# Kernel optimization log

Hardware: AMD Instinct MI355X
Metric: run time of the kernel (lower is better)

## Reference

```python
import jax, jax.numpy as jnp
import numpy as np

DIN = 128
HID = 128
B, N = 32, 2048
NEG = 9000000000000000.0


def setup_inputs() -> dict:
    key = jax.random.key(0)
    ks = jax.random.split(key, 8)
    x = jax.random.normal(ks[0], (B, N, DIN), dtype=jnp.float32)
    mask = jax.random.randint(ks[1], (B, N, N), 0, 2).astype(jnp.float32)
    s = 1.0 / np.sqrt(DIN)
    Wv = jax.random.uniform(ks[2], (DIN, HID), minval=-s, maxval=s, dtype=jnp.float32)
    bv = jax.random.uniform(ks[3], (HID,), minval=-s, maxval=s, dtype=jnp.float32)
    Wk = jax.random.uniform(ks[4], (DIN, HID), minval=-s, maxval=s, dtype=jnp.float32)
    bk = jax.random.uniform(ks[5], (HID,), minval=-s, maxval=s, dtype=jnp.float32)
    Wq = jax.random.uniform(ks[6], (DIN, HID), minval=-s, maxval=s, dtype=jnp.float32)
    bq = jax.random.uniform(ks[7], (HID,), minval=-s, maxval=s, dtype=jnp.float32)
    return {"x": x, "mask": mask, "Wv": Wv, "bv": bv, "Wk": Wk, "bk": bk, "Wq": Wq, "bq": bq}


def reference(x, mask, Wv, bv, Wk, bk, Wq, bq):
    v = jnp.tanh(x @ Wv + bv)            # [B, N, H]
    q = jnp.tanh(x @ Wq + bq)            # [B, N, H]
    k = jnp.tanh(x @ Wk + bk)            # [B, N, H]
    scores = jnp.einsum('bih,bjh->bij', q, k)  # [B, N, N]
    scores = scores * mask - NEG * (1.0 - mask)
    att = jax.nn.softmax(scores, axis=-1)
    out = jnp.einsum('bij,bjh->bih', att, v)   # [B, N, H]
    return out
```

## Files before the change

### kernel.cpp

```cpp
#include <hip/hip_runtime.h>

#define DIN 128
#define HID 128
#define BB  32
#define NN  2048
#define LOG2E 1.44269504088896340736f

typedef float  f32x4   __attribute__((ext_vector_type(4)));
typedef __bf16 bf16x4v __attribute__((ext_vector_type(4)));
typedef __bf16 bf16x8  __attribute__((ext_vector_type(8)));

__device__ __forceinline__ float tanh_fast(float x) {
  float e = __expf(2.0f * x);
  return 1.0f - 2.0f / (e + 1.0f);
}

__global__ __launch_bounds__(256) void wt_kernel(
    const float* __restrict__ Wq, const float* __restrict__ Wk,
    const float* __restrict__ Wv, __bf16* __restrict__ wt) {
  const float* W = (blockIdx.x == 0) ? Wq : (blockIdx.x == 1) ? Wk : Wv;
  __bf16* dst = wt + blockIdx.x * (DIN * HID);
  int t = threadIdx.x;
#pragma unroll
  for (int c = 0; c < 16; ++c) {
    int o = c * 1024 + t * 4;
    int d = o >> 7, h = o & 127;
    f32x4 v = *(const f32x4*)(W + d * HID + h);
    dst[(h + 0) * DIN + d] = (__bf16)v.x;
    dst[(h + 1) * DIN + d] = (__bf16)v.y;
    dst[(h + 2) * DIN + d] = (__bf16)v.z;
    dst[(h + 3) * DIN + d] = (__bf16)v.w;
  }
}

__global__ __launch_bounds__(256) void proj_kernel(
    const float* __restrict__ x, const __bf16* __restrict__ wt,
    const float* __restrict__ bq, const float* __restrict__ bk,
    const float* __restrict__ bv, __bf16* __restrict__ qbf,
    __bf16* __restrict__ kbf, __bf16* __restrict__ vtbf) {
  int tid = threadIdx.x;
  int lane = tid & 63, w = tid >> 6;
  int l15 = lane & 15, quad = lane >> 4;
  long i0 = (long)blockIdx.x * 64;

  bf16x8 bx[4][4];
#pragma unroll
  for (int nt = 0; nt < 4; ++nt) {
    const float* xp = x + (i0 + nt * 16 + l15) * DIN;
#pragma unroll
    for (int ks = 0; ks < 4; ++ks) {
      int d0 = ks * 32 + quad * 8;
      f32x4 a = *(const f32x4*)(xp + d0);
      f32x4 b = *(const f32x4*)(xp + d0 + 4);
      bf16x8 f;
      f[0] = (__bf16)a.x; f[1] = (__bf16)a.y; f[2] = (__bf16)a.z; f[3] = (__bf16)a.w;
      f[4] = (__bf16)b.x; f[5] = (__bf16)b.y; f[6] = (__bf16)b.z; f[7] = (__bf16)b.w;
      bx[nt][ks] = f;
    }
  }

#pragma unroll
  for (int p = 0; p < 2; ++p) {
    const __bf16* wtp = wt + p * DIN * HID;
    const float* bias = (p == 0) ? bq : bk;
    __bf16* outp = (p == 0) ? qbf : kbf;
#pragma unroll
    for (int nt = 0; nt < 8; ++nt) {
      int h0 = nt * 16 + l15;
      f32x4 acc = {0.f, 0.f, 0.f, 0.f};
#pragma unroll
      for (int ks = 0; ks < 4; ++ks) {
        bf16x8 wf = *(const bf16x8*)(wtp + (long)h0 * DIN + ks * 32 + quad * 8);
        acc = __builtin_amdgcn_mfma_f32_16x16x32_bf16(bx[w][ks], wf, acc, 0, 0, 0);
      }
      float bcol = bias[h0];
      long rowb = i0 + w * 16 + quad * 4;
#pragma unroll
      for (int r = 0; r < 4; ++r) {
        float val = tanh_fast(acc[r] + bcol);
        if (p == 0) val *= LOG2E;
        outp[(rowb + r) * HID + h0] = (__bf16)val;
      }
    }
  }

  {
    const __bf16* wtp = wt + 2 * DIN * HID;
    long bb = i0 >> 11;
    int nloc = (int)(i0 & 2047);
    long vbase = bb * (long)HID * NN;
#pragma unroll
    for (int s = 0; s < 2; ++s) {
      int hb = w * 32 + s * 16;
      bf16x8 af[4];
#pragma unroll
      for (int ks = 0; ks < 4; ++ks)
        af[ks] = *(const bf16x8*)(wtp + (long)(hb + l15) * DIN + ks * 32 + quad * 8);
      float bvr[4];
#pragma unroll
      for (int r = 0; r < 4; ++r) bvr[r] = bv[hb + quad * 4 + r];
#pragma unroll
      for (int nt = 0; nt < 4; ++nt) {
        f32x4 acc = {0.f, 0.f, 0.f, 0.f};
#pragma unroll
        for (int ks = 0; ks < 4; ++ks)
          acc = __builtin_amdgcn_mfma_f32_16x16x32_bf16(af[ks], bx[nt][ks], acc, 0, 0, 0);
        int hrow = hb + quad * 4;
        int ncol = nloc + nt * 16 + l15;
#pragma unroll
        for (int r = 0; r < 4; ++r) {
          float val = tanh_fast(acc[r] + bvr[r]);
          vtbf[vbase + (long)(hrow + r) * NN + ncol] = (__bf16)val;
        }
      }
    }
  }
}

#define KSTR 136
#define VSTR 72
#define PSTR 72

__global__ __launch_bounds__(512, 4) void attn_kernel(
    const __bf16* __restrict__ qbf, const __bf16* __restrict__ kbf,
    const __bf16* __restrict__ vtbf, const float* __restrict__ mask,
    float* __restrict__ out) {
  __shared__ __bf16 Ks[64 * KSTR];
  __shared__ __bf16 Vts[128 * VSTR];
  __shared__ __bf16 Pl[8 * 16 * PSTR];

  const int tid = threadIdx.x;
  const int lane = tid & 63, w = tid >> 6;
  const int l15 = lane & 15, quad = lane >> 4;
  const int bid = blockIdx.x;
  const int vb = (bid >> 3) | ((bid & 7) << 6);
  const int b = vb >> 4;
  const int i0 = (vb & 15) * 128;
  const long kvbase = (long)b * NN * HID;

  bf16x8 qf[4];
  {
    const __bf16* qp = qbf + kvbase + (long)(i0 + w * 16 + l15) * HID + quad * 8;
#pragma unroll
    for (int ks = 0; ks < 4; ++ks) qf[ks] = *(const bf16x8*)(qp + ks * 32);
  }

  const int krow = tid >> 4, kcol = (tid & 15) * 8;
  const int vrow = tid >> 3, vcol = (tid & 7) * 8;
  const __bf16* kg = kbf + kvbase + (long)krow * HID + kcol;
  const __bf16* vg = vtbf + (long)b * HID * NN + (long)vrow * NN + vcol;
  __bf16* ksd0 = Ks + krow * KSTR + kcol;
  __bf16* ksd1 = Ks + (krow + 32) * KSTR + kcol;
  __bf16* vsd0 = Vts + vrow * VSTR + vcol;
  __bf16* vsd1 = Vts + (vrow + 64) * VSTR + vcol;
  const float* mp = mask + ((long)b * NN + (i0 + w * 16 + l15)) * NN + quad * 4;
  __bf16* Pw = Pl + w * 16 * PSTR;

  f32x4 O[8];
#pragma unroll
  for (int i = 0; i < 8; ++i) O[i] = (f32x4){0.f, 0.f, 0.f, 0.f};
  float mrow = -1e30f, lrow = 0.0f;

  bf16x8 kr0 = *(const bf16x8*)(kg);
  bf16x8 kr1 = *(const bf16x8*)(kg + 32 * HID);
  bf16x8 vr0 = *(const bf16x8*)(vg);
  bf16x8 vr1 = *(const bf16x8*)(vg + (long)64 * NN);
  f32x4 mr[4];
#pragma unroll
  for (int t = 0; t < 4; ++t) mr[t] = *(const f32x4*)(mp + t * 16);
  *(bf16x8*)ksd0 = kr0; *(bf16x8*)ksd1 = kr1;
  *(bf16x8*)vsd0 = vr0; *(bf16x8*)vsd1 = vr1;
  unsigned mbits;
  {
    float mb = 0.f;
#pragma unroll
    for (int t = 0; t < 4; ++t)
#pragma unroll
      for (int r = 0; r < 4; ++r)
        mb = fmaf(mr[t][r], (float)(1u << (t * 4 + r)), mb);
    mbits = (unsigned)mb;
  }
  __syncthreads();

  for (int jt = 0; jt < 32; ++jt) {
    const int jn = (jt < 31) ? jt + 1 : 31;
    {
      const __bf16* kgn = kg + (long)jn * 64 * HID;
      kr0 = *(const bf16x8*)(kgn);
      kr1 = *(const bf16x8*)(kgn + 32 * HID);
      const __bf16* vgn = vg + jn * 64;
      vr0 = *(const bf16x8*)(vgn);
      vr1 = *(const bf16x8*)(vgn + (long)64 * NN);
#pragma unroll
      for (int t = 0; t < 4; ++t) mr[t] = *(const f32x4*)(mp + jn * 64 + t * 16);
    }

    f32x4 pt[4];
#pragma unroll
    for (int t = 0; t < 4; ++t) {
      f32x4 acc = {0.f, 0.f, 0.f, 0.f};
      const __bf16* kp = Ks + (t * 16 + l15) * KSTR + quad * 8;
#pragma unroll
      for (int ks = 0; ks < 4; ++ks) {
        bf16x8 kf = *(const bf16x8*)(kp + ks * 32);
        acc = __builtin_amdgcn_mfma_f32_16x16x32_bf16(kf, qf[ks], acc, 0, 0, 0);
      }
      pt[t] = acc;
    }

    float tmx = -1e30f;
#pragma unroll
    for (int t = 0; t < 4; ++t)
#pragma unroll
      for (int r = 0; r < 4; ++r) {
        float s = ((mbits >> (t * 4 + r)) & 1u) ? pt[t][r] : -1e30f;
        pt[t][r] = s;
        tmx = fmaxf(tmx, s);
      }
    tmx = fmaxf(tmx, __shfl_xor(tmx, 16));
    tmx = fmaxf(tmx, __shfl_xor(tmx, 32));
    const float mnew = fmaxf(mrow, tmx);
    const float alpha = exp2f(mrow - mnew);
    float rs = 0.0f;
#pragma unroll
    for (int t = 0; t < 4; ++t)
#pragma unroll
      for (int r = 0; r < 4; ++r) {
        float p = exp2f(pt[t][r] - mnew);
        pt[t][r] = p;
        rs += p;
      }
    rs += __shfl_xor(rs, 16);
    rs += __shfl_xor(rs, 32);
    lrow = lrow * alpha + rs;
    mrow = mnew;

    float ar[4];
#pragma unroll
    for (int r = 0; r < 4; ++r) ar[r] = __shfl(alpha, (quad << 2) + r);
#pragma unroll
    for (int nt = 0; nt < 8; ++nt)
#pragma unroll
      for (int r = 0; r < 4; ++r) O[nt][r] *= ar[r];

#pragma unroll
    for (int t = 0; t < 4; ++t) {
      bf16x4v pb;
#pragma unroll
      for (int r = 0; r < 4; ++r) pb[r] = (__bf16)pt[t][r];
      *(bf16x4v*)(Pw + l15 * PSTR + t * 16 + quad * 4) = pb;
    }
    const bf16x8 pf0 = *(const bf16x8*)(Pw + l15 * PSTR + quad * 8);
    const bf16x8 pf1 = *(const bf16x8*)(Pw + l15 * PSTR + 32 + quad * 8);

#pragma unroll
    for (int nt = 0; nt < 8; ++nt) {
      const __bf16* vp = Vts + (nt * 16 + l15) * VSTR + quad * 8;
      bf16x8 vf0 = *(const bf16x8*)(vp);
      bf16x8 vf1 = *(const bf16x8*)(vp + 32);
      O[nt] = __builtin_amdgcn_mfma_f32_16x16x32_bf16(pf0, vf0, O[nt], 0, 0, 0);
      O[nt] = __builtin_amdgcn_mfma_f32_16x16x32_bf16(pf1, vf1, O[nt], 0, 0, 0);
    }

    __syncthreads();
    *(bf16x8*)ksd0 = kr0; *(bf16x8*)ksd1 = kr1;
    *(bf16x8*)vsd0 = vr0; *(bf16x8*)vsd1 = vr1;
    {
      float mb = 0.f;
#pragma unroll
      for (int t = 0; t < 4; ++t)
#pragma unroll
        for (int r = 0; r < 4; ++r)
          mb = fmaf(mr[t][r], (float)(1u << (t * 4 + r)), mb);
      mbits = (unsigned)mb;
    }
    __syncthreads();
  }

  const float inv = 1.0f / lrow;
  float il[4];
#pragma unroll
  for (int r = 0; r < 4; ++r) il[r] = __shfl(inv, (quad << 2) + r);
  const long rowb = (long)b * NN + i0 + w * 16 + quad * 4;
#pragma unroll
  for (int r = 0; r < 4; ++r) {
    float* op = out + (rowb + r) * HID;
#pragma unroll
    for (int nt = 0; nt < 8; ++nt) op[nt * 16 + l15] = O[nt][r] * il[r];
  }
}

extern "C" void kernel_launch(void* const* d_in, const int* in_sizes, int n_in,
                              void* d_out, int out_size, void* d_ws, size_t ws_size,
                              hipStream_t stream) {
  const float* x    = (const float*)d_in[0];
  const float* mask = (const float*)d_in[1];
  const float* Wv   = (const float*)d_in[2];
  const float* bv   = (const float*)d_in[3];
  const float* Wk   = (const float*)d_in[4];
  const float* bk   = (const float*)d_in[5];
  const float* Wq   = (const float*)d_in[6];
  const float* bq   = (const float*)d_in[7];
  float* out = (float*)d_out;

  __bf16* ws = (__bf16*)d_ws;
  __bf16* wt   = ws;
  __bf16* qbf  = ws + 3 * DIN * HID;
  __bf16* kbf  = qbf + (long)BB * NN * HID;
  __bf16* vtbf = kbf + (long)BB * NN * HID;

  wt_kernel<<<3, 256, 0, stream>>>(Wq, Wk, Wv, wt);
  proj_kernel<<<BB * NN / 64, 256, 0, stream>>>(x, wt, bq, bk, bv, qbf, kbf, vtbf);
  attn_kernel<<<512, 512, 0, stream>>>(qbf, kbf, vtbf, mask, out);
}
```

Before: 842.6 us.

## Precompute packed mask bits in projection kernel and skip unneeded rescales

The projection kernel now also reads the fp32 mask once and packs it into a bitmask of one bit per element, stored in workspace. The attention kernel then loads one 64-bit word per row per key tile instead of four float4 vectors, and no longer builds the bits with float FMAs inside its loop. Separately, the running-output rescale is skipped when no row maximum in the wavefront grew. In exchange, proj_kernel gains a large streaming pass over the mask plus an extra workspace write and read, and the rescale skip adds a wave vote and a branch.

```diff
diff --git a/kernel.cpp b/kernel.cpp
--- a/kernel.cpp
+++ b/kernel.cpp
@@ -36,8 +36,9 @@
 __global__ __launch_bounds__(256) void proj_kernel(
     const float* __restrict__ x, const __bf16* __restrict__ wt,
     const float* __restrict__ bq, const float* __restrict__ bk,
-    const float* __restrict__ bv, __bf16* __restrict__ qbf,
-    __bf16* __restrict__ kbf, __bf16* __restrict__ vtbf) {
+    const float* __restrict__ bv, const float* __restrict__ mask,
+    __bf16* __restrict__ qbf, __bf16* __restrict__ kbf,
+    __bf16* __restrict__ vtbf, unsigned* __restrict__ mbits) {
   int tid = threadIdx.x;
   int lane = tid & 63, w = tid >> 6;
   int l15 = lane & 15, quad = lane >> 4;
@@ -115,6 +116,24 @@
       }
     }
   }
+
+  {
+    for (int it = 0; it < 16; ++it) {
+      int gid = it * 256 + tid;
+      int r = gid >> 6, j = gid & 63;
+      const float* p = mask + (i0 + r) * NN + j * 32;
+      unsigned bits = 0;
+#pragma unroll
+      for (int c = 0; c < 8; ++c) {
+        f32x4 v = *(const f32x4*)(p + c * 4);
+        bits |= (v.x != 0.f ? 1u : 0u) << (c * 4 + 0);
+        bits |= (v.y != 0.f ? 1u : 0u) << (c * 4 + 1);
+        bits |= (v.z != 0.f ? 1u : 0u) << (c * 4 + 2);
+        bits |= (v.w != 0.f ? 1u : 0u) << (c * 4 + 3);
+      }
+      mbits[(i0 + r) * 64 + j] = bits;
+    }
+  }
 }
 
 #define KSTR 136
@@ -123,7 +142,7 @@
 
 __global__ __launch_bounds__(512, 4) void attn_kernel(
     const __bf16* __restrict__ qbf, const __bf16* __restrict__ kbf,
-    const __bf16* __restrict__ vtbf, const float* __restrict__ mask,
+    const __bf16* __restrict__ vtbf, const unsigned* __restrict__ mbits,
     float* __restrict__ out) {
   __shared__ __bf16 Ks[64 * KSTR];
   __shared__ __bf16 Vts[128 * VSTR];
@@ -153,7 +172,7 @@
   __bf16* ksd1 = Ks + (krow + 32) * KSTR + kcol;
   __bf16* vsd0 = Vts + vrow * VSTR + vcol;
   __bf16* vsd1 = Vts + (vrow + 64) * VSTR + vcol;
-  const float* mp = mask + ((long)b * NN + (i0 + w * 16 + l15)) * NN + quad * 4;
+  const unsigned* mrp = mbits + ((long)b * NN + (i0 + w * 16 + l15)) * 64;
   __bf16* Pw = Pl + w * 16 * PSTR;
 
   f32x4 O[8];
@@ -165,25 +184,14 @@
   bf16x8 kr1 = *(const bf16x8*)(kg + 32 * HID);
   bf16x8 vr0 = *(const bf16x8*)(vg);
   bf16x8 vr1 = *(const bf16x8*)(vg + (long)64 * NN);
-  f32x4 mr[4];
-#pragma unroll
-  for (int t = 0; t < 4; ++t) mr[t] = *(const f32x4*)(mp + t * 16);
+  unsigned long long mw = *(const unsigned long long*)(mrp);
   *(bf16x8*)ksd0 = kr0; *(bf16x8*)ksd1 = kr1;
   *(bf16x8*)vsd0 = vr0; *(bf16x8*)vsd1 = vr1;
-  unsigned mbits;
-  {
-    float mb = 0.f;
-#pragma unroll
-    for (int t = 0; t < 4; ++t)
-#pragma unroll
-      for (int r = 0; r < 4; ++r)
-        mb = fmaf(mr[t][r], (float)(1u << (t * 4 + r)), mb);
-    mbits = (unsigned)mb;
-  }
   __syncthreads();
 
   for (int jt = 0; jt < 32; ++jt) {
     const int jn = (jt < 31) ? jt + 1 : 31;
+    unsigned long long mwn;
     {
       const __bf16* kgn = kg + (long)jn * 64 * HID;
       kr0 = *(const bf16x8*)(kgn);
@@ -191,8 +199,7 @@
       const __bf16* vgn = vg + jn * 64;
       vr0 = *(const bf16x8*)(vgn);
       vr1 = *(const bf16x8*)(vgn + (long)64 * NN);
-#pragma unroll
-      for (int t = 0; t < 4; ++t) mr[t] = *(const f32x4*)(mp + jn * 64 + t * 16);
+      mwn = *(const unsigned long long*)(mrp + jn * 2);
     }
 
     f32x4 pt[4];
@@ -208,17 +215,23 @@
       pt[t] = acc;
     }
 
+    unsigned mb16 = 0;
+#pragma unroll
+    for (int t = 0; t < 4; ++t)
+      mb16 |= ((unsigned)(mw >> (t * 16 + (quad << 2))) & 0xFu) << (t * 4);
+
     float tmx = -1e30f;
 #pragma unroll
     for (int t = 0; t < 4; ++t)
 #pragma unroll
       for (int r = 0; r < 4; ++r) {
-        float s = ((mbits >> (t * 4 + r)) & 1u) ? pt[t][r] : -1e30f;
+        float s = ((mb16 >> (t * 4 + r)) & 1u) ? pt[t][r] : -1e30f;
         pt[t][r] = s;
         tmx = fmaxf(tmx, s);
       }
     tmx = fmaxf(tmx, __shfl_xor(tmx, 16));
     tmx = fmaxf(tmx, __shfl_xor(tmx, 32));
+    const bool grow = !__all(tmx <= mrow);
     const float mnew = fmaxf(mrow, tmx);
     const float alpha = exp2f(mrow - mnew);
     float rs = 0.0f;
@@ -235,13 +248,15 @@
     lrow = lrow * alpha + rs;
     mrow = mnew;
 
-    float ar[4];
-#pragma unroll
-    for (int r = 0; r < 4; ++r) ar[r] = __shfl(alpha, (quad << 2) + r);
-#pragma unroll
-    for (int nt = 0; nt < 8; ++nt)
-#pragma unroll
-      for (int r = 0; r < 4; ++r) O[nt][r] *= ar[r];
+    if (grow) {
+      float ar[4];
+#pragma unroll
+      for (int r = 0; r < 4; ++r) ar[r] = __shfl(alpha, (quad << 2) + r);
+#pragma unroll
+      for (int nt = 0; nt < 8; ++nt)
+#pragma unroll
+        for (int r = 0; r < 4; ++r) O[nt][r] *= ar[r];
+    }
 
 #pragma unroll
     for (int t = 0; t < 4; ++t) {
@@ -265,15 +280,7 @@
     __syncthreads();
     *(bf16x8*)ksd0 = kr0; *(bf16x8*)ksd1 = kr1;
     *(bf16x8*)vsd0 = vr0; *(bf16x8*)vsd1 = vr1;
-    {
-      float mb = 0.f;
-#pragma unroll
-      for (int t = 0; t < 4; ++t)
-#pragma unroll
-        for (int r = 0; r < 4; ++r)
-          mb = fmaf(mr[t][r], (float)(1u << (t * 4 + r)), mb);
-      mbits = (unsigned)mb;
-    }
+    mw = mwn;
     __syncthreads();
   }
 
@@ -308,8 +315,10 @@
   __bf16* qbf  = ws + 3 * DIN * HID;
   __bf16* kbf  = qbf + (long)BB * NN * HID;
   __bf16* vtbf = kbf + (long)BB * NN * HID;
+  unsigned* mbits = (unsigned*)(vtbf + (long)BB * NN * HID);
 
   wt_kernel<<<3, 256, 0, stream>>>(Wq, Wk, Wv, wt);
-  proj_kernel<<<BB * NN / 64, 256, 0, stream>>>(x, wt, bq, bk, bv, qbf, kbf, vtbf);
-  attn_kernel<<<512, 512, 0, stream>>>(qbf, kbf, vtbf, mask, out);
-}
+  proj_kernel<<<BB * NN / 64, 256, 0, stream>>>(x, wt, bq, bk, bv, mask,
+                                                qbf, kbf, vtbf, mbits);
+  attn_kernel<<<512, 512, 0, stream>>>(qbf, kbf, vtbf, mbits, out);
+}
```

Measured after the change: 921.5 us. +9.4%, slower.

## Double-buffer K/V tiles in LDS with XOR swizzle and skip redundant rescale

Applied to the files above, without the earlier changes.

K and V^T tiles are now double-buffered in shared memory, so the next tile is stored into the alternate buffer. This removes one __syncthreads per iteration. Padded strides are replaced by an XOR swizzle to avoid bank conflicts, and the P staging area reuses the wave's slice of the idle K buffer. The output rescale by alpha is skipped when no row max grew in the wave. Risks include 64KB of LDS per block, which may limit occupancy, plus extra address arithmetic and a wave-wide vote per tile.

```diff
diff --git a/kernel.cpp b/kernel.cpp
--- a/kernel.cpp
+++ b/kernel.cpp
@@ -117,21 +117,17 @@
   }
 }
 
-#define KSTR 136
-#define VSTR 72
-#define PSTR 72
-
 __global__ __launch_bounds__(512, 4) void attn_kernel(
     const __bf16* __restrict__ qbf, const __bf16* __restrict__ kbf,
     const __bf16* __restrict__ vtbf, const float* __restrict__ mask,
     float* __restrict__ out) {
-  __shared__ __bf16 Ks[64 * KSTR];
-  __shared__ __bf16 Vts[128 * VSTR];
-  __shared__ __bf16 Pl[8 * 16 * PSTR];
+  __shared__ __bf16 Ks[2][64 * 128];
+  __shared__ __bf16 Vts[2][128 * 64];
 
   const int tid = threadIdx.x;
   const int lane = tid & 63, w = tid >> 6;
   const int l15 = lane & 15, quad = lane >> 4;
+  const int swz = (l15 & 7) << 3;
   const int bid = blockIdx.x;
   const int vb = (bid >> 3) | ((bid & 7) << 6);
   const int b = vb >> 4;
@@ -145,16 +141,17 @@
     for (int ks = 0; ks < 4; ++ks) qf[ks] = *(const bf16x8*)(qp + ks * 32);
   }
 
-  const int krow = tid >> 4, kcol = (tid & 15) * 8;
-  const int vrow = tid >> 3, vcol = (tid & 7) * 8;
-  const __bf16* kg = kbf + kvbase + (long)krow * HID + kcol;
-  const __bf16* vg = vtbf + (long)b * HID * NN + (long)vrow * NN + vcol;
-  __bf16* ksd0 = Ks + krow * KSTR + kcol;
-  __bf16* ksd1 = Ks + (krow + 32) * KSTR + kcol;
-  __bf16* vsd0 = Vts + vrow * VSTR + vcol;
-  __bf16* vsd1 = Vts + (vrow + 64) * VSTR + vcol;
+  const int krl = (w << 3) + (lane >> 3);
+  const int kcl = (lane & 7) * 8;
+  const int vrl = (w << 4) + (lane >> 2);
+  const int vcl = (lane & 3) * 8;
+  const __bf16* kg = kbf + kvbase + (long)krl * HID + kcl;
+  const __bf16* vg = vtbf + (long)b * HID * NN + (long)vrl * NN + vcl;
+  const int ksw0 = krl * 128 + (kcl ^ ((krl & 7) << 3));
+  const int ksw1 = krl * 128 + ((kcl + 64) ^ ((krl & 7) << 3));
+  const int vsw0 = vrl * 64 + (vcl ^ ((vrl & 7) << 3));
+  const int vsw1 = vrl * 64 + ((vcl + 32) ^ ((vrl & 7) << 3));
   const float* mp = mask + ((long)b * NN + (i0 + w * 16 + l15)) * NN + quad * 4;
-  __bf16* Pw = Pl + w * 16 * PSTR;
 
   f32x4 O[8];
 #pragma unroll
@@ -162,14 +159,14 @@
   float mrow = -1e30f, lrow = 0.0f;
 
   bf16x8 kr0 = *(const bf16x8*)(kg);
-  bf16x8 kr1 = *(const bf16x8*)(kg + 32 * HID);
+  bf16x8 kr1 = *(const bf16x8*)(kg + 64);
   bf16x8 vr0 = *(const bf16x8*)(vg);
-  bf16x8 vr1 = *(const bf16x8*)(vg + (long)64 * NN);
+  bf16x8 vr1 = *(const bf16x8*)(vg + 32);
   f32x4 mr[4];
 #pragma unroll
   for (int t = 0; t < 4; ++t) mr[t] = *(const f32x4*)(mp + t * 16);
-  *(bf16x8*)ksd0 = kr0; *(bf16x8*)ksd1 = kr1;
-  *(bf16x8*)vsd0 = vr0; *(bf16x8*)vsd1 = vr1;
+  *(bf16x8*)&Ks[0][ksw0] = kr0; *(bf16x8*)&Ks[0][ksw1] = kr1;
+  *(bf16x8*)&Vts[0][vsw0] = vr0; *(bf16x8*)&Vts[0][vsw1] = vr1;
   unsigned mbits;
   {
     float mb = 0.f;
@@ -182,15 +179,16 @@
   }
   __syncthreads();
 
+  int cur = 0;
   for (int jt = 0; jt < 32; ++jt) {
     const int jn = (jt < 31) ? jt + 1 : 31;
     {
       const __bf16* kgn = kg + (long)jn * 64 * HID;
       kr0 = *(const bf16x8*)(kgn);
-      kr1 = *(const bf16x8*)(kgn + 32 * HID);
+      kr1 = *(const bf16x8*)(kgn + 64);
       const __bf16* vgn = vg + jn * 64;
       vr0 = *(const bf16x8*)(vgn);
-      vr1 = *(const bf16x8*)(vgn + (long)64 * NN);
+      vr1 = *(const bf16x8*)(vgn + 32);
 #pragma unroll
       for (int t = 0; t < 4; ++t) mr[t] = *(const f32x4*)(mp + jn * 64 + t * 16);
     }
@@ -199,10 +197,10 @@
 #pragma unroll
     for (int t = 0; t < 4; ++t) {
       f32x4 acc = {0.f, 0.f, 0.f, 0.f};
-      const __bf16* kp = Ks + (t * 16 + l15) * KSTR + quad * 8;
+      const int krow = t * 16 + l15;
 #pragma unroll
       for (int ks = 0; ks < 4; ++ks) {
-        bf16x8 kf = *(const bf16x8*)(kp + ks * 32);
+        bf16x8 kf = *(const bf16x8*)&Ks[cur][krow * 128 + ((quad * 8 + ks * 32) ^ swz)];
         acc = __builtin_amdgcn_mfma_f32_16x16x32_bf16(kf, qf[ks], acc, 0, 0, 0);
       }
       pt[t] = acc;
@@ -219,6 +217,7 @@
       }
     tmx = fmaxf(tmx, __shfl_xor(tmx, 16));
     tmx = fmaxf(tmx, __shfl_xor(tmx, 32));
+    const bool grow = !__all(tmx <= mrow);
     const float mnew = fmaxf(mrow, tmx);
     const float alpha = exp2f(mrow - mnew);
     float rs = 0.0f;
@@ -235,36 +234,38 @@
     lrow = lrow * alpha + rs;
     mrow = mnew;
 
-    float ar[4];
-#pragma unroll
-    for (int r = 0; r < 4; ++r) ar[r] = __shfl(alpha, (quad << 2) + r);
-#pragma unroll
-    for (int nt = 0; nt < 8; ++nt)
-#pragma unroll
-      for (int r = 0; r < 4; ++r) O[nt][r] *= ar[r];
-
+    if (grow) {
+      float ar[4];
+#pragma unroll
+      for (int r = 0; r < 4; ++r) ar[r] = __shfl(alpha, (quad << 2) + r);
+#pragma unroll
+      for (int nt = 0; nt < 8; ++nt)
+#pragma unroll
+        for (int r = 0; r < 4; ++r) O[nt][r] *= ar[r];
+    }
+
+    __bf16* Pw = &Ks[cur ^ 1][w * 1024];
 #pragma unroll
     for (int t = 0; t < 4; ++t) {
       bf16x4v pb;
 #pragma unroll
       for (int r = 0; r < 4; ++r) pb[r] = (__bf16)pt[t][r];
-      *(bf16x4v*)(Pw + l15 * PSTR + t * 16 + quad * 4) = pb;
-    }
-    const bf16x8 pf0 = *(const bf16x8*)(Pw + l15 * PSTR + quad * 8);
-    const bf16x8 pf1 = *(const bf16x8*)(Pw + l15 * PSTR + 32 + quad * 8);
+      *(bf16x4v*)&Pw[l15 * 64 + ((t * 16 + quad * 4) ^ swz)] = pb;
+    }
+    const bf16x8 pf0 = *(const bf16x8*)&Pw[l15 * 64 + ((quad * 8) ^ swz)];
+    const bf16x8 pf1 = *(const bf16x8*)&Pw[l15 * 64 + ((quad * 8 + 32) ^ swz)];
 
 #pragma unroll
     for (int nt = 0; nt < 8; ++nt) {
-      const __bf16* vp = Vts + (nt * 16 + l15) * VSTR + quad * 8;
-      bf16x8 vf0 = *(const bf16x8*)(vp);
-      bf16x8 vf1 = *(const bf16x8*)(vp + 32);
+      const int vrow = nt * 16 + l15;
+      bf16x8 vf0 = *(const bf16x8*)&Vts[cur][vrow * 64 + ((quad * 8) ^ swz)];
+      bf16x8 vf1 = *(const bf16x8*)&Vts[cur][vrow * 64 + ((quad * 8 + 32) ^ swz)];
       O[nt] = __builtin_amdgcn_mfma_f32_16x16x32_bf16(pf0, vf0, O[nt], 0, 0, 0);
       O[nt] = __builtin_amdgcn_mfma_f32_16x16x32_bf16(pf1, vf1, O[nt], 0, 0, 0);
     }
 
-    __syncthreads();
-    *(bf16x8*)ksd0 = kr0; *(bf16x8*)ksd1 = kr1;
-    *(bf16x8*)vsd0 = vr0; *(bf16x8*)vsd1 = vr1;
+    *(bf16x8*)&Ks[cur ^ 1][ksw0] = kr0; *(bf16x8*)&Ks[cur ^ 1][ksw1] = kr1;
+    *(bf16x8*)&Vts[cur ^ 1][vsw0] = vr0; *(bf16x8*)&Vts[cur ^ 1][vsw1] = vr1;
     {
       float mb = 0.f;
 #pragma unroll
@@ -275,6 +276,7 @@
       mbits = (unsigned)mb;
     }
     __syncthreads();
+    cur ^= 1;
   }
 
   const float inv = 1.0f / lrow;
```

Result: slower. 893.3 us (+6.0%).
